# Kernel tuning notes

Measured on AMD Instinct MI355X. Metric: run time of the kernel, lower is better.

The kernel has to match this reference:

```python
import jax, jax.numpy as jnp
import numpy as np

N = 100000   # nodes
E = 1600000  # edges
F_IN = 128
H = 128
C = 20


def setup_inputs() -> dict:
    key = jax.random.key(0)
    ks = jax.random.split(key, 12)
    s = lambda k, sh: jax.random.normal(k, sh, dtype=jnp.float32) * 0.05
    return {
        "x": jax.random.normal(ks[0], (N, F_IN), dtype=jnp.float32),
        "edge_index": jax.random.randint(ks[1], (2, E), 0, N, dtype=jnp.int64),
        # SAGEConv1: lin_l (neighbor, with bias), lin_r (root, no bias)
        "W1l": s(ks[2], (H, F_IN)), "b1": jnp.zeros((H,), jnp.float32), "W1r": s(ks[3], (H, F_IN)),
        # SAGEConv2
        "W2l": s(ks[4], (H, H)), "b2": jnp.zeros((H,), jnp.float32), "W2r": s(ks[5], (H, H)),
        # MLP head
        "Wm1": s(ks[6], (H, H)), "bm1": jnp.zeros((H,), jnp.float32),
        "Wm2": s(ks[7], (C, H)), "bm2": jnp.zeros((C,), jnp.float32),
    }


def _sage_conv(x, src, dst, Wl, bl, Wr):
    # PyG SAGEConv (aggr='mean'): out = lin_l(mean_{j in N(i)} x_j) + lin_r(x_i)
    msg = x[src]                                             # [E, d] irregular gather
    agg = jax.ops.segment_sum(msg, dst, num_segments=N)      # [N, d] scatter-add
    cnt = jax.ops.segment_sum(jnp.ones((msg.shape[0], 1), x.dtype), dst, num_segments=N)
    mean = agg / jnp.maximum(cnt, 1.0)
    return mean @ Wl.T + bl + x @ Wr.T


def reference(x, edge_index, W1l, b1, W1r, W2l, b2, W2r, Wm1, bm1, Wm2, bm2):
    src, dst = edge_index[0], edge_index[1]
    # two SAGEConv layers, each followed by relu (dropout = identity at eval)
    h = jax.nn.relu(_sage_conv(x, src, dst, W1l, b1, W1r))
    h = jax.nn.relu(_sage_conv(h, src, dst, W2l, b2, W2r))
    # MLP: Linear -> dropout(identity) -> ReLU -> Linear, then sigmoid
    h = jax.nn.relu(h @ Wm1.T + bm1)
    return jax.nn.sigmoid(h @ Wm2.T + bm2)
```

## Files before the change

### kernel.cpp

```cpp
#include <hip/hip_runtime.h>
#include <math.h>

#define NODES 100000
#define EDGES 1600000
#define HF 128
#define NC 20
#define CAPN 64
#define BSHIFT 8
#define BNODES 256
#define NBK ((NODES + BNODES - 1) / BNODES)
#define CAP 4608
#define EPB 16384
#define NPB ((EDGES + EPB - 1) / EPB)
#define XB ((NODES * HF / 8 + 255) / 256)

typedef __attribute__((ext_vector_type(8))) short bf16x8;
typedef __attribute__((ext_vector_type(4))) float f32x4;
typedef __attribute__((ext_vector_type(2))) float f32x2;

__device__ __forceinline__ ushort f2b(float f) {
    uint u = __float_as_uint(f);
    uint r = (u + 0x7FFFu + ((u >> 16) & 1u)) >> 16;
    return (ushort)r;
}
__device__ __forceinline__ uchar f2q(float f) {
    return (uchar)(__builtin_amdgcn_cvt_pk_fp8_f32(f, f, 0, false) & 0xFF);
}

__global__ void prep_kernel(const float* __restrict__ x, ushort* __restrict__ xb,
                            uchar* __restrict__ xq,
                            const float* __restrict__ a, const float* __restrict__ b,
                            const float* __restrict__ c, const float* __restrict__ d,
                            const float* __restrict__ e, const float* __restrict__ wm2,
                            ushort* __restrict__ wb,
                            const int* __restrict__ src, const int* __restrict__ dst,
                            int* __restrict__ bcur, uint* __restrict__ ebufp,
                            int n8, int E) {
    __shared__ int h[NBK];
    __shared__ int basea[NBK];
    int blk = blockIdx.x;
    int t = threadIdx.x;
    if (blk < NPB) {
        int base = blk * EPB;
        const int4* d4 = (const int4*)(dst + base);
        const int4* s4 = (const int4*)(src + base);
        for (int i = t; i < NBK; i += 256) h[i] = 0;
        __syncthreads();
#pragma unroll
        for (int it = 0; it < EPB / 1024; ++it) {
            int i4 = it * 256 + t;
            if (base + i4 * 4 < E) {
                int4 dv = d4[i4];
                atomicAdd(&h[dv.x >> BSHIFT], 1);
                atomicAdd(&h[dv.y >> BSHIFT], 1);
                atomicAdd(&h[dv.z >> BSHIFT], 1);
                atomicAdd(&h[dv.w >> BSHIFT], 1);
            }
        }
        __syncthreads();
        for (int i = t; i < NBK; i += 256) {
            int cc = h[i];
            basea[i] = cc ? (i * CAP + atomicAdd(&bcur[i], cc)) : 0;
        }
        __syncthreads();
        for (int i = t; i < NBK; i += 256) h[i] = 0;
        __syncthreads();
#pragma unroll
        for (int it = 0; it < EPB / 1024; ++it) {
            int i4 = it * 256 + t;
            if (base + i4 * 4 < E) {
                int4 dv = d4[i4];
                int4 sv = s4[i4];
                const int dd[4] = {dv.x, dv.y, dv.z, dv.w};
                const int ss[4] = {sv.x, sv.y, sv.z, sv.w};
#pragma unroll
                for (int k = 0; k < 4; ++k) {
                    int bb = dd[k] >> BSHIFT;
                    int pos = basea[bb] + atomicAdd(&h[bb], 1);
                    ebufp[pos] = ((uint)(dd[k] & (BNODES - 1)) << 17) | (uint)ss[k];
                }
            }
        }
    } else if (blk < NPB + XB) {
        int i = (blk - NPB) * 256 + t;
        if (i >= n8) return;
        const float4* p = (const float4*)x + (size_t)i * 2;
        float4 va = p[0], vb = p[1];
        uint4 o;
        o.x = (uint)f2b(va.x) | ((uint)f2b(va.y) << 16);
        o.y = (uint)f2b(va.z) | ((uint)f2b(va.w) << 16);
        o.z = (uint)f2b(vb.x) | ((uint)f2b(vb.y) << 16);
        o.w = (uint)f2b(vb.z) | ((uint)f2b(vb.w) << 16);
        ((uint4*)xb)[i] = o;
        uint2 q;
        q.x = __builtin_amdgcn_cvt_pk_fp8_f32(va.x, va.y, 0, false);
        q.x = __builtin_amdgcn_cvt_pk_fp8_f32(va.z, va.w, q.x, true);
        q.y = __builtin_amdgcn_cvt_pk_fp8_f32(vb.x, vb.y, 0, false);
        q.y = __builtin_amdgcn_cvt_pk_fp8_f32(vb.z, vb.w, q.y, true);
        ((uint2*)xq)[i] = q;
    } else {
        int i = (blk - NPB - XB) * 256 + t;
        if (i < 81920) {
            const float* srcs[5] = {a, b, c, d, e};
            wb[i] = f2b(srcs[i >> 14][i & 16383]);
        } else if (i < 86016) {
            int j = i - 81920;
            wb[i] = ((j >> 7) < NC) ? f2b(wm2[j]) : (ushort)0;
        }
    }
}

__global__ void csr_build(const uint* __restrict__ ebufp, const int* __restrict__ bcur,
                          int* __restrict__ cnt, int* __restrict__ ssrcp) {
    __shared__ int lcnt[BNODES];
    int b = blockIdx.x;
    int t = threadIdx.x;
    lcnt[t] = 0;
    __syncthreads();
    int e0 = b * CAP;
    int cb = bcur[b];
    int nbase = b << BSHIFT;
    const uint4* e4 = (const uint4*)(ebufp + e0);
    int n4 = (cb + 3) >> 2;
    for (int i4 = t; i4 < n4; i4 += 256) {
        uint4 ev = e4[i4];
        const uint ee[4] = {ev.x, ev.y, ev.z, ev.w};
        int base4 = i4 * 4;
#pragma unroll
        for (int k = 0; k < 4; ++k) {
            if (base4 + k < cb) {
                int loc = (int)(ee[k] >> 17);
                int sv = (int)(ee[k] & 0x1FFFFu);
                int slot = atomicAdd(&lcnt[loc], 1);
                if (slot < CAPN)
                    ssrcp[(size_t)(nbase + loc) * CAPN + slot] = sv;
            }
        }
    }
    __syncthreads();
    int node = nbase + t;
    if (node < NODES) cnt[node] = lcnt[t];
}

template<bool EMITQ, bool FUSE>
__global__ __launch_bounds__(512)
void fused_sage_layer(const uchar* __restrict__ Xq, const ushort* __restrict__ X,
                      const int* __restrict__ ssrcp, const int* __restrict__ cnt,
                      const ushort* __restrict__ Wl, const ushort* __restrict__ Wr,
                      const float* __restrict__ bias, ushort* __restrict__ out,
                      uchar* __restrict__ outq,
                      const ushort* __restrict__ Wm1b, const ushort* __restrict__ Wm2b,
                      const float* __restrict__ bm1, const float* __restrict__ bm2,
                      float* __restrict__ fout, int n) {
    __shared__ ushort sh[64][136];
    __shared__ int sidx[64 * CAPN];
    __shared__ int s_len[64];
    int row0b = blockIdx.x * 64;
    int t = threadIdx.x;

    if (t < 64) {
        int node = row0b + t;
        s_len[t] = (node < n) ? min(cnt[node], CAPN) : 0;
    }
    int nrows = min(64, n - row0b);
    int lim = nrows * CAPN;
    const int* wsrc = ssrcp + (size_t)row0b * CAPN;
    for (int i = t; i < lim; i += 512) sidx[i] = wsrc[i] << 7;
    __syncthreads();

    {
        int grp = t >> 5;
        int sub = t & 31;
        int sel = sub >> 3;
        int cg = sub & 7;
        const uchar* xc = Xq + cg * 16;
#pragma unroll
        for (int batch = 0; batch < 4; ++batch) {
            int nloc = batch * 16 + grp;
            int node = row0b + nloc;
            int len = s_len[nloc];
            int sbase = nloc * CAPN;
            f32x2 acc2[8];
#pragma unroll
            for (int i = 0; i < 8; ++i) acc2[i] = f32x2{0.f, 0.f};
            for (int e = 0; e < len; e += 16) {
                uint4 v[4];
#pragma unroll
                for (int w = 0; w < 4; ++w) {
                    int ee = e + 4 * w + sel;
                    int off = sidx[sbase + ee];
                    uint4 vv = {0u, 0u, 0u, 0u};
                    if (ee < len) vv = *(const uint4*)(xc + (size_t)(uint)off);
                    v[w] = vv;
                }
#pragma unroll
                for (int w = 0; w < 4; ++w) {
                    const uint* pp = (const uint*)&v[w];
#pragma unroll
                    for (int i = 0; i < 4; ++i) {
                        acc2[2 * i]     += __builtin_amdgcn_cvt_pk_f32_fp8(pp[i], false);
                        acc2[2 * i + 1] += __builtin_amdgcn_cvt_pk_f32_fp8(pp[i], true);
                    }
                }
            }
#pragma unroll
            for (int i = 0; i < 8; ++i) {
                acc2[i].x += __shfl_xor(acc2[i].x, 8);
                acc2[i].x += __shfl_xor(acc2[i].x, 16);
                acc2[i].y += __shfl_xor(acc2[i].y, 8);
                acc2[i].y += __shfl_xor(acc2[i].y, 16);
            }
            if (sel == 0 && node < n) {
                float invd = 1.0f / fmaxf((float)len, 1.0f);
                uint4 o0, o1;
                uint* p0 = (uint*)&o0;
                uint* p1 = (uint*)&o1;
#pragma unroll
                for (int i = 0; i < 4; ++i) {
                    p0[i] = (uint)f2b(acc2[i].x * invd) | ((uint)f2b(acc2[i].y * invd) << 16);
                    p1[i] = (uint)f2b(acc2[4 + i].x * invd) | ((uint)f2b(acc2[4 + i].y * invd) << 16);
                }
                *(uint4*)(&sh[nloc][cg * 16]) = o0;
                *(uint4*)(&sh[nloc][cg * 16 + 8]) = o1;
            }
        }
    }
    __syncthreads();

    int wave = t >> 6;
    int lane = t & 63;
    int m = lane & 15, quad = lane >> 4;
    int col = wave * 16 + m;

    bf16x8 bl[4], br[4];
#pragma unroll
    for (int ks = 0; ks < 4; ++ks) {
        bl[ks] = *(const bf16x8*)(Wl + (size_t)col * HF + ks * 32 + quad * 8);
        br[ks] = *(const bf16x8*)(Wr + (size_t)col * HF + ks * 32 + quad * 8);
    }
    float bia = bias[col];

    if (!FUSE) {
#pragma unroll
        for (int rt = 0; rt < 4; ++rt) {
            int row0 = row0b + rt * 16;
            if (row0 >= n) break;
            f32x4 acc = {0.f, 0.f, 0.f, 0.f};
            const ushort* arow = X + (size_t)(row0 + m) * HF + quad * 8;
#pragma unroll
            for (int ks = 0; ks < 4; ++ks) {
                bf16x8 a = *(const bf16x8*)(&sh[rt * 16 + m][ks * 32 + quad * 8]);
                acc = __builtin_amdgcn_mfma_f32_16x16x32_bf16(a, bl[ks], acc, 0, 0, 0);
                bf16x8 ar = *(const bf16x8*)(arow + ks * 32);
                acc = __builtin_amdgcn_mfma_f32_16x16x32_bf16(ar, br[ks], acc, 0, 0, 0);
            }
#pragma unroll
            for (int i = 0; i < 4; ++i) {
                int r = row0 + quad * 4 + i;
                if (r < n) {
                    float v = fmaxf(acc[i] + bia, 0.f);
                    out[(size_t)r * HF + col] = f2b(v);
                    if (EMITQ) outq[(size_t)r * HF + col] = f2q(v);
                }
            }
        }
    } else {
        f32x4 accs[4];
#pragma unroll
        for (int rt = 0; rt < 4; ++rt) {
            int row0 = row0b + rt * 16;
            f32x4 acc = {0.f, 0.f, 0.f, 0.f};
            if (row0 < n) {
                const ushort* arow = X + (size_t)(row0 + m) * HF + quad * 8;
#pragma unroll
                for (int ks = 0; ks < 4; ++ks) {
                    bf16x8 a = *(const bf16x8*)(&sh[rt * 16 + m][ks * 32 + quad * 8]);
                    acc = __builtin_amdgcn_mfma_f32_16x16x32_bf16(a, bl[ks], acc, 0, 0, 0);
                    bf16x8 ar = *(const bf16x8*)(arow + ks * 32);
                    acc = __builtin_amdgcn_mfma_f32_16x16x32_bf16(ar, br[ks], acc, 0, 0, 0);
                }
            }
            accs[rt] = acc;
        }
        __syncthreads();
#pragma unroll
        for (int rt = 0; rt < 4; ++rt)
#pragma unroll
            for (int i = 0; i < 4; ++i)
                sh[rt * 16 + quad * 4 + i][col] = f2b(fmaxf(accs[rt][i] + bia, 0.f));
        __syncthreads();

        bf16x8 w1[4];
#pragma unroll
        for (int ks = 0; ks < 4; ++ks)
            w1[ks] = *(const bf16x8*)(Wm1b + (size_t)col * HF + ks * 32 + quad * 8);
        float hb = bm1[col];
        f32x4 hacc[4];
#pragma unroll
        for (int rt = 0; rt < 4; ++rt) {
            f32x4 acc = {0.f, 0.f, 0.f, 0.f};
#pragma unroll
            for (int ks = 0; ks < 4; ++ks) {
                bf16x8 a = *(const bf16x8*)(&sh[rt * 16 + m][ks * 32 + quad * 8]);
                acc = __builtin_amdgcn_mfma_f32_16x16x32_bf16(a, w1[ks], acc, 0, 0, 0);
            }
            hacc[rt] = acc;
        }
        __syncthreads();
#pragma unroll
        for (int rt = 0; rt < 4; ++rt)
#pragma unroll
            for (int i = 0; i < 4; ++i)
                sh[rt * 16 + quad * 4 + i][col] = f2b(fmaxf(hacc[rt][i] + hb, 0.f));
        __syncthreads();

        if (wave < 4) {
            bf16x8 c0f[4], c1f[4];
#pragma unroll
            for (int ks = 0; ks < 4; ++ks) {
                c0f[ks] = *(const bf16x8*)(Wm2b + (size_t)m * HF + ks * 32 + quad * 8);
                c1f[ks] = *(const bf16x8*)(Wm2b + (size_t)(16 + m) * HF + ks * 32 + quad * 8);
            }
            f32x4 o0 = {0.f, 0.f, 0.f, 0.f};
            f32x4 o1 = {0.f, 0.f, 0.f, 0.f};
#pragma unroll
            for (int ks = 0; ks < 4; ++ks) {
                bf16x8 a = *(const bf16x8*)(&sh[wave * 16 + m][ks * 32 + quad * 8]);
                o0 = __builtin_amdgcn_mfma_f32_16x16x32_bf16(a, c0f[ks], o0, 0, 0, 0);
                o1 = __builtin_amdgcn_mfma_f32_16x16x32_bf16(a, c1f[ks], o1, 0, 0, 0);
            }
            float bb0 = bm2[m];
            float bb1 = (m < 4) ? bm2[16 + m] : 0.f;
#pragma unroll
            for (int i = 0; i < 4; ++i) {
                int row = row0b + wave * 16 + quad * 4 + i;
                if (row < n) {
                    fout[(size_t)row * NC + m] = 1.0f / (1.0f + expf(-(o0[i] + bb0)));
                    if (m < 4)
                        fout[(size_t)row * NC + 16 + m] = 1.0f / (1.0f + expf(-(o1[i] + bb1)));
                }
            }
        }
    }
}

extern "C" void kernel_launch(void* const* d_in, const int* in_sizes, int n_in,
                              void* d_out, int out_size, void* d_ws, size_t ws_size,
                              hipStream_t stream) {
    const float* x   = (const float*)d_in[0];
    const int*   ei  = (const int*)d_in[1];
    const float* W1l = (const float*)d_in[2];
    const float* b1  = (const float*)d_in[3];
    const float* W1r = (const float*)d_in[4];
    const float* W2l = (const float*)d_in[5];
    const float* b2  = (const float*)d_in[6];
    const float* W2r = (const float*)d_in[7];
    const float* Wm1 = (const float*)d_in[8];
    const float* bm1 = (const float*)d_in[9];
    const float* Wm2 = (const float*)d_in[10];
    const float* bm2 = (const float*)d_in[11];
    float* out = (float*)d_out;

    const int N = NODES, E = EDGES;
    const int* src = ei;
    const int* dst = ei + E;

    int* cnt    = (int*)d_ws;
    int* bcur   = cnt + 100352;
    int* ssrcp  = bcur + 512;
    ushort* xb  = (ushort*)(ssrcp + (size_t)N * CAPN);
    ushort* h1  = xb + (size_t)N * HF;
    uint* ebufp = (uint*)h1;
    ushort* wb  = h1 + (size_t)N * HF;
    uchar* xq   = (uchar*)(wb + 86016);
    uchar* h1q  = xq + (size_t)N * HF;
    ushort* wb1l = wb;
    ushort* wb1r = wb + 16384;
    ushort* wb2l = wb + 32768;
    ushort* wb2r = wb + 49152;
    ushort* wbm1 = wb + 65536;
    ushort* wbm2 = wb + 81920;

    const int n8 = N * HF / 8;

    hipMemsetAsync(bcur, 0, 512 * sizeof(int), stream);
    prep_kernel<<<NPB + XB + 336, 256, 0, stream>>>(
        x, xb, xq, W1l, W1r, W2l, W2r, Wm1, Wm2, wb, src, dst, bcur, ebufp, n8, E);
    csr_build<<<NBK, 256, 0, stream>>>(ebufp, bcur, cnt, ssrcp);

    const int fusedBlocks = (N + 63) / 64;

    fused_sage_layer<true, false><<<fusedBlocks, 512, 0, stream>>>(
        xq, xb, ssrcp, cnt, wb1l, wb1r, b1, h1, h1q,
        nullptr, nullptr, nullptr, nullptr, nullptr, N);
    fused_sage_layer<false, true><<<fusedBlocks, 512, 0, stream>>>(
        h1q, h1, ssrcp, cnt, wb2l, wb2r, b2, nullptr, nullptr,
        wbm1, wbm2, bm1, bm2, out, N);
}
```

Measured before the change: 309.6 us.

## Fuse CSR build into SAGE layers by bucketing edges per 64-node block

Shrinks edge buckets to 64 nodes so each bucket matches one fused-layer block, and drops the separate csr_build kernel. Each layer kernel now reads its bucket of packed edges and builds the per-node neighbor lists in shared memory with LDS atomics. This removes one launch and the padded N*64 ssrcp write and read. In exchange the bucketing is redone in both layers, neighbor order becomes nondeterministic, and edges beyond CAPB per bucket are dropped.

```diff
diff --git a/kernel.cpp b/kernel.cpp
--- a/kernel.cpp
+++ b/kernel.cpp
@@ -6,10 +6,10 @@
 #define HF 128
 #define NC 20
 #define CAPN 64
-#define BSHIFT 8
-#define BNODES 256
+#define BSHIFT 6
+#define BNODES 64
 #define NBK ((NODES + BNODES - 1) / BNODES)
-#define CAP 4608
+#define CAPB 1280
 #define EPB 16384
 #define NPB ((EDGES + EPB - 1) / EPB)
 #define XB ((NODES * HF / 8 + 255) / 256)
@@ -60,7 +60,7 @@
         __syncthreads();
         for (int i = t; i < NBK; i += 256) {
             int cc = h[i];
-            basea[i] = cc ? (i * CAP + atomicAdd(&bcur[i], cc)) : 0;
+            basea[i] = cc ? (i * CAPB + atomicAdd(&bcur[i], cc)) : 0;
         }
         __syncthreads();
         for (int i = t; i < NBK; i += 256) h[i] = 0;
@@ -77,7 +77,8 @@
                 for (int k = 0; k < 4; ++k) {
                     int bb = dd[k] >> BSHIFT;
                     int pos = basea[bb] + atomicAdd(&h[bb], 1);
-                    ebufp[pos] = ((uint)(dd[k] & (BNODES - 1)) << 17) | (uint)ss[k];
+                    if (pos < (bb + 1) * CAPB)
+                        ebufp[pos] = ((uint)(dd[k] & (BNODES - 1)) << 17) | (uint)ss[k];
                 }
             }
         }
@@ -110,42 +111,10 @@
     }
 }
 
-__global__ void csr_build(const uint* __restrict__ ebufp, const int* __restrict__ bcur,
-                          int* __restrict__ cnt, int* __restrict__ ssrcp) {
-    __shared__ int lcnt[BNODES];
-    int b = blockIdx.x;
-    int t = threadIdx.x;
-    lcnt[t] = 0;
-    __syncthreads();
-    int e0 = b * CAP;
-    int cb = bcur[b];
-    int nbase = b << BSHIFT;
-    const uint4* e4 = (const uint4*)(ebufp + e0);
-    int n4 = (cb + 3) >> 2;
-    for (int i4 = t; i4 < n4; i4 += 256) {
-        uint4 ev = e4[i4];
-        const uint ee[4] = {ev.x, ev.y, ev.z, ev.w};
-        int base4 = i4 * 4;
-#pragma unroll
-        for (int k = 0; k < 4; ++k) {
-            if (base4 + k < cb) {
-                int loc = (int)(ee[k] >> 17);
-                int sv = (int)(ee[k] & 0x1FFFFu);
-                int slot = atomicAdd(&lcnt[loc], 1);
-                if (slot < CAPN)
-                    ssrcp[(size_t)(nbase + loc) * CAPN + slot] = sv;
-            }
-        }
-    }
-    __syncthreads();
-    int node = nbase + t;
-    if (node < NODES) cnt[node] = lcnt[t];
-}
-
 template<bool EMITQ, bool FUSE>
 __global__ __launch_bounds__(512)
 void fused_sage_layer(const uchar* __restrict__ Xq, const ushort* __restrict__ X,
-                      const int* __restrict__ ssrcp, const int* __restrict__ cnt,
+                      const uint* __restrict__ ebufp, const int* __restrict__ bcur,
                       const ushort* __restrict__ Wl, const ushort* __restrict__ Wr,
                       const float* __restrict__ bias, ushort* __restrict__ out,
                       uchar* __restrict__ outq,
@@ -154,18 +123,21 @@
                       float* __restrict__ fout, int n) {
     __shared__ ushort sh[64][136];
     __shared__ int sidx[64 * CAPN];
-    __shared__ int s_len[64];
+    __shared__ int lcnt[64];
     int row0b = blockIdx.x * 64;
     int t = threadIdx.x;
 
-    if (t < 64) {
-        int node = row0b + t;
-        s_len[t] = (node < n) ? min(cnt[node], CAPN) : 0;
-    }
-    int nrows = min(64, n - row0b);
-    int lim = nrows * CAPN;
-    const int* wsrc = ssrcp + (size_t)row0b * CAPN;
-    for (int i = t; i < lim; i += 512) sidx[i] = wsrc[i] << 7;
+    if (t < 64) lcnt[t] = 0;
+    __syncthreads();
+    int cb = min(bcur[blockIdx.x], CAPB);
+    const uint* ep = ebufp + (size_t)blockIdx.x * CAPB;
+    for (int i = t; i < cb; i += 512) {
+        uint e = ep[i];
+        int loc = (int)(e >> 17);
+        int slot = atomicAdd(&lcnt[loc], 1);
+        if (slot < CAPN)
+            sidx[loc * CAPN + slot] = (int)((e & 0x1FFFFu) << 7);
+    }
     __syncthreads();
 
     {
@@ -178,7 +150,7 @@
         for (int batch = 0; batch < 4; ++batch) {
             int nloc = batch * 16 + grp;
             int node = row0b + nloc;
-            int len = s_len[nloc];
+            int len = min(lcnt[nloc], CAPN);
             int sbase = nloc * CAPN;
             f32x2 acc2[8];
 #pragma unroll
@@ -365,12 +337,10 @@
     const int* src = ei;
     const int* dst = ei + E;
 
-    int* cnt    = (int*)d_ws;
-    int* bcur   = cnt + 100352;
-    int* ssrcp  = bcur + 512;
-    ushort* xb  = (ushort*)(ssrcp + (size_t)N * CAPN);
+    int* bcur   = (int*)d_ws;
+    uint* ebufp = (uint*)(bcur + 1568);
+    ushort* xb  = (ushort*)(ebufp + (size_t)NBK * CAPB);
     ushort* h1  = xb + (size_t)N * HF;
-    uint* ebufp = (uint*)h1;
     ushort* wb  = h1 + (size_t)N * HF;
     uchar* xq   = (uchar*)(wb + 86016);
     uchar* h1q  = xq + (size_t)N * HF;
@@ -383,17 +353,16 @@
 
     const int n8 = N * HF / 8;
 
-    hipMemsetAsync(bcur, 0, 512 * sizeof(int), stream);
+    hipMemsetAsync(bcur, 0, NBK * sizeof(int), stream);
     prep_kernel<<<NPB + XB + 336, 256, 0, stream>>>(
         x, xb, xq, W1l, W1r, W2l, W2r, Wm1, Wm2, wb, src, dst, bcur, ebufp, n8, E);
-    csr_build<<<NBK, 256, 0, stream>>>(ebufp, bcur, cnt, ssrcp);
 
     const int fusedBlocks = (N + 63) / 64;
 
     fused_sage_layer<true, false><<<fusedBlocks, 512, 0, stream>>>(
-        xq, xb, ssrcp, cnt, wb1l, wb1r, b1, h1, h1q,
+        xq, xb, ebufp, bcur, wb1l, wb1r, b1, h1, h1q,
         nullptr, nullptr, nullptr, nullptr, nullptr, N);
     fused_sage_layer<false, true><<<fusedBlocks, 512, 0, stream>>>(
-        h1q, h1, ssrcp, cnt, wb2l, wb2r, b2, nullptr, nullptr,
+        h1q, h1, ebufp, bcur, wb2l, wb2r, b2, nullptr, nullptr,
         wbm1, wbm2, bm1, bm2, out, N);
 }
```

Result: faster. 290.7 us (-6.1%).
